# Optimization experiments

Hardware: AMD Instinct MI355X
Metric: run time of the kernel (lower is better)

The kernel has to match this reference:

```python
import jax, jax.numpy as jnp
import numpy as np

BN_EPS = 1e-5


def setup_inputs() -> dict:
    key = jax.random.key(0)
    ks = jax.random.split(key, 9)
    b, c, h, w = 8, 256, 256, 25
    p2_r = jax.random.normal(ks[0], (b, c, h, w), dtype=jnp.float32)
    # message-passing conv weight; scaled so the 25-step recurrence stays bounded
    W_msg = jax.random.normal(ks[1], (256, 256, 1, 9), dtype=jnp.float32) * 0.02
    bn_gamma = jax.random.uniform(ks[2], (256,), dtype=jnp.float32, minval=0.5, maxval=1.5)
    bn_beta = jax.random.normal(ks[3], (256,), dtype=jnp.float32) * 0.1
    bn_mean = jax.random.normal(ks[4], (256,), dtype=jnp.float32) * 0.1
    bn_var = jax.random.uniform(ks[5], (256,), dtype=jnp.float32, minval=0.5, maxval=1.5)
    W_up2 = jax.random.normal(ks[6], (256, 256, 3, 3), dtype=jnp.float32) * (1.0 / np.sqrt(256 * 9))
    W_conv = jax.random.normal(ks[7], (1, 256, 1, 1), dtype=jnp.float32) * (1.0 / np.sqrt(256))
    W_conv2 = jax.random.normal(ks[8], (1, 25, 1, 1), dtype=jnp.float32) * (1.0 / np.sqrt(25))
    return {"p2_r": p2_r, "W_msg": W_msg, "bn_gamma": bn_gamma, "bn_beta": bn_beta,
            "bn_mean": bn_mean, "bn_var": bn_var, "W_up2": W_up2,
            "W_conv": W_conv, "W_conv2": W_conv2}


def r_scnn(x, Wc, reverse):
    # x: [b,c,h,w]. The (1,9) conv with padding (0,4) on width-1 slices only
    # touches the kernel's center tap -> per-step 256x256 matvec recurrence.
    xs = jnp.moveaxis(x, 3, 0)  # [w,b,c,h]
    if reverse:
        xs = xs[::-1]

    def step(carry, xi):
        new = xi + jax.nn.relu(jnp.einsum('oc,bch->boh', Wc, carry))
        return new, new

    _, rest = jax.lax.scan(step, xs[0], xs[1:])
    out = jnp.concatenate([xs[:1], rest], axis=0)[::-1]  # source reverses output order
    return jnp.moveaxis(out, 0, 3)  # [b,c,h,w]


def batchnorm(x, gamma, beta, mean, var):
    inv = gamma / jnp.sqrt(var + BN_EPS)
    return x * inv[None, :, None, None] + (beta - mean * inv)[None, :, None, None]


def upsample_h2(x):
    # bilinear, align_corners=True, size=(2H, W): only height doubles
    b, c, H, W = x.shape
    nh = 2 * H
    pos = jnp.arange(nh, dtype=jnp.float32) * ((H - 1) / (nh - 1))
    i0 = jnp.floor(pos).astype(jnp.int32)
    i1 = jnp.minimum(i0 + 1, H - 1)
    t = (pos - i0.astype(jnp.float32))[None, None, :, None]
    return x[:, :, i0, :] * (1.0 - t) + x[:, :, i1, :] * t


def reference(p2_r, W_msg, bn_gamma, bn_beta, bn_mean, bn_var, W_up2, W_conv, W_conv2):
    Wc = W_msg[:, :, 0, 4]  # effective center tap of the (1,9) conv
    x = r_scnn(p2_r, Wc, reverse=False)
    x = jax.nn.relu(batchnorm(x, bn_gamma, bn_beta, bn_mean, bn_var))
    x = r_scnn(x, Wc, reverse=True)
    x = jax.nn.relu(batchnorm(x, bn_gamma, bn_beta, bn_mean, bn_var))
    x = upsample_h2(x)  # [b,256,2h,w]
    x = jax.lax.conv_general_dilated(x, W_up2, (1, 1), ((1, 1), (1, 1)),
                                     dimension_numbers=('NCHW', 'OIHW', 'NCHW'))
    x = upsample_h2(x)  # [b,256,4h,w]
    x = jnp.einsum('oc,bchw->bohw', W_conv[:, :, 0, 0], x)  # 1x1 conv 256->1
    x = upsample_h2(x)  # [b,1,8h,w]
    x = jnp.swapaxes(x, 1, 3)  # [b,w,8h,1]
    x = jnp.einsum('oc,bchw->bohw', W_conv2[:, :, 0, 0], x)  # 1x1 conv 25->1
    return jax.nn.sigmoid(x)  # [b,1,8h,1]
```

## Files before the change

### kernel.cpp

```cpp
#include <hip/hip_runtime.h>
#include <math.h>


#define NC 8

typedef __attribute__((ext_vector_type(8))) short bf16x8;
typedef __attribute__((ext_vector_type(4))) float f32x4;

__device__ __forceinline__ float relu_(float v) { return fmaxf(v, 0.f); }

__device__ __forceinline__ short f2bf(float f) {
  union { float f; unsigned u; } v; v.f = f;
  unsigned r = (v.u + 0x7fffu + ((v.u >> 16) & 1u)) >> 16;
  return (short)r;
}
__device__ __forceinline__ float bf2f(short s) {
  union { unsigned u; float f; } v;
  v.u = ((unsigned)(unsigned short)s) << 16;
  return v.f;
}
__device__ __forceinline__ unsigned cvtpk(float lo, float hi) {
  unsigned r;
  asm("v_cvt_pk_bf16_f32 %0, %1, %2" : "=v"(r) : "v"(lo), "v"(hi));
  return r;
}
__device__ __forceinline__ float dpp_xor8(float v) {
  int r = __builtin_amdgcn_update_dpp(0, __float_as_int(v), 0x128, 0xf, 0xf, true);
  return __int_as_float(r);
}

__global__ __launch_bounds__(64) void k0_precompute(
    const float* __restrict__ Wmsg, const float* __restrict__ gamma,
    const float* __restrict__ beta, const float* __restrict__ mean,
    const float* __restrict__ var, const float* __restrict__ Wup2,
    const float* __restrict__ Wconv, const float* __restrict__ Wconv2,
    short* __restrict__ WcA, float* __restrict__ A, float* __restrict__ bnp)
{
  const int c = blockIdx.x;
  const int lane = threadIdx.x;

  for (int o = lane; o < 256; o += 64)
    WcA[o * 256 + c] = f2bf(Wmsg[(o * 256 + c) * 9 + 4]);

  const int gtid = c * 64 + lane;
  if (gtid < 256) {
    float inv = gamma[gtid] / sqrtf(var[gtid] + 1e-5f);
    bnp[gtid] = inv;
    bnp[256 + gtid] = beta[gtid] - mean[gtid] * inv;
  }

  float wacc[9];
#pragma unroll
  for (int q = 0; q < 9; ++q) wacc[q] = 0.f;
  for (int o = lane; o < 256; o += 64) {
    float cw = Wconv[o];
    const float* wp = Wup2 + (size_t)(o * 256 + c) * 9;
#pragma unroll
    for (int q = 0; q < 9; ++q) wacc[q] += cw * wp[q];
  }
#pragma unroll
  for (int q = 0; q < 9; ++q) {
    float v = wacc[q];
    v += __shfl_xor(v, 32, 64);
    v += __shfl_xor(v, 16, 64);
    v += __shfl_xor(v, 8, 64);
    v += __shfl_xor(v, 4, 64);
    v += __shfl_xor(v, 2, 64);
    v += __shfl_xor(v, 1, 64);
    wacc[q] = v;
  }
  if (lane == 0) {
    for (int dh = 0; dh < 3; ++dh)
      for (int j = 0; j < 25; ++j) {
        float a = 0.f;
        for (int dw = 0; dw < 3; ++dw) {
          int w = j + 1 - dw;
          if (w >= 0 && w < 25) a += wacc[dh * 3 + dw] * Wconv2[w];
        }
        A[(dh * 25 + j) * 256 + c] = a;
      }
  }
}

__global__ __launch_bounds__(512, 1) void k2_fused(
    const float* __restrict__ X,
    const short* __restrict__ WcA,
    const float* __restrict__ A,
    const float* __restrict__ bnp,
    float* __restrict__ S)
{
  __shared__ short xslab[25 * 8 * 256];
  __shared__ short yz[2][16 * 256];
  __shared__ float red[8][8][3];
  const int tid = threadIdx.x;
  const int wave = tid >> 6;
  const int lane = tid & 63;
  const int n = lane & 15;
  const int nr = n & 7;
  const int g = lane >> 4;
  const bool isz = (n >= 8);
  const int col0 = blockIdx.x * NC;
  const int b = col0 >> 8, h0 = col0 & 255;
  const int obase = wave * 32;
  char* xs = (char*)xslab;
  char* smem = (char*)yz;

  if (lane < 50) {
    int base_[4], sx_[4];
#pragma unroll
    for (int e = 0; e < 4; ++e) {
      int f = 4 * lane + e;
      int rn = f / 25, w = f - rn * 25;
      base_[e] = w * 4096 + rn * 512;
      sx_[e] = ((2 * rn + w) & 15) << 3;
    }
    const float* src0 = X + (size_t)(b * 256 + obase) * 6400 + h0 * 25 + 4 * lane;
#pragma unroll 4
    for (int i = 0; i < 16; ++i) {
      float4 v0 = *(const float4*)(src0 + (size_t)(2 * i) * 6400);
      float4 v1 = *(const float4*)(src0 + (size_t)(2 * i + 1) * 6400);
      unsigned p[4] = {cvtpk(v0.x, v1.x), cvtpk(v0.y, v1.y),
                       cvtpk(v0.z, v1.z), cvtpk(v0.w, v1.w)};
      const int cb = 2 * obase + 4 * i;
#pragma unroll
      for (int e = 0; e < 4; ++e)
        *(unsigned*)(xs + base_[e] + (cb ^ sx_[e])) = p[e];
    }
  }

  f32x4 inv[2], addv[2];
#pragma unroll
  for (int t = 0; t < 2; ++t) {
    inv[t] = *(const f32x4*)(bnp + obase + t * 16 + g * 4);
    addv[t] = *(const f32x4*)(bnp + 256 + obase + t * 16 + g * 4);
  }

  bf16x8 af[2][8];
#pragma unroll
  for (int t = 0; t < 2; ++t)
#pragma unroll
    for (int kk = 0; kk < 8; ++kk)
      af[t][kk] = *(const bf16x8*)(WcA + (obase + t * 16 + n) * 256 + kk * 32 + g * 8);

  const int swz = nr << 4;
  int woff[2], xb[2], roff[8];
#pragma unroll
  for (int t = 0; t < 2; ++t) {
    woff[t] = n * 512 + (((obase + t * 16 + g * 4) * 2) ^ swz);
    xb[t] = nr * 512 + 2 * (obase + t * 16 + g * 4);
  }
#pragma unroll
  for (int kk = 0; kk < 8; ++kk)
    roff[kk] = n * 512 + ((kk * 64 + g * 16) ^ swz);

  __syncthreads();

  {
    const int S0 = ((2 * nr) & 15) << 3;
#pragma unroll
    for (int t = 0; t < 2; ++t) {
      uint2 xq0 = *(const uint2*)(xs + (xb[t] ^ S0));
      if (!isz) {
        *(uint2*)(smem + woff[t]) = xq0;
      } else {
        float zr[4], t2r[4];
        float xv[4] = {bf2f((short)xq0.x), bf2f((short)(xq0.x >> 16)),
                       bf2f((short)xq0.y), bf2f((short)(xq0.y >> 16))};
#pragma unroll
        for (int r = 0; r < 4; ++r) {
          zr[r] = relu_(xv[r] * inv[t][r] + addv[t][r]);
          t2r[r] = relu_(zr[r] * inv[t][r] + addv[t][r]);
        }
        *(uint2*)(smem + woff[t]) = make_uint2(cvtpk(zr[0], zr[1]), cvtpk(zr[2], zr[3]));
        *(uint2*)(xs + (xb[t] ^ S0)) =
            make_uint2(cvtpk(t2r[0], t2r[1]), cvtpk(t2r[2], t2r[3]));
      }
    }
  }

  uint2 xq[2];
  xq[0] = make_uint2(0u, 0u);
  xq[1] = make_uint2(0u, 0u);
  if (!isz) {
    const int S1 = ((2 * nr + 1) & 15) << 3;
#pragma unroll
    for (int t = 0; t < 2; ++t)
      xq[t] = *(const uint2*)(xs + ((xb[t] + 4096) ^ S1));
  }
  __syncthreads();

#pragma unroll 1
  for (int k = 1; k < 25; ++k) {
    const int cur = (k - 1) & 1, nxt = k & 1;

    bf16x8 bfr[8];
#pragma unroll
    for (int kk = 0; kk < 8; ++kk)
      bfr[kk] = *(const bf16x8*)(smem + cur * 8192 + roff[kk]);

    f32x4 accA[2], accB[2];
#pragma unroll
    for (int t = 0; t < 2; ++t) {
      accA[t] = (f32x4){0.f, 0.f, 0.f, 0.f};
      accB[t] = (f32x4){0.f, 0.f, 0.f, 0.f};
    }
    __builtin_amdgcn_s_setprio(1);
#pragma unroll
    for (int kk = 0; kk < 4; ++kk)
#pragma unroll
      for (int t = 0; t < 2; ++t)
        accA[t] = __builtin_amdgcn_mfma_f32_16x16x32_bf16(af[t][kk], bfr[kk], accA[t], 0, 0, 0);
#pragma unroll
    for (int kk = 4; kk < 8; ++kk)
#pragma unroll
      for (int t = 0; t < 2; ++t)
        accB[t] = __builtin_amdgcn_mfma_f32_16x16x32_bf16(af[t][kk], bfr[kk], accB[t], 0, 0, 0);
    __builtin_amdgcn_s_setprio(0);

    float cyv[2][4], ynv[2][4], t1v[2][4], t1s[2][4];
#pragma unroll
    for (int t = 0; t < 2; ++t) {
      f32x4 acc = accA[t] + accB[t];
      float xv[4];
      xv[0] = bf2f((short)xq[t].x);
      xv[1] = bf2f((short)(xq[t].x >> 16));
      xv[2] = bf2f((short)xq[t].y);
      xv[3] = bf2f((short)(xq[t].y >> 16));
#pragma unroll
      for (int r = 0; r < 4; ++r) {
        cyv[t][r] = relu_(acc[r]);
        ynv[t][r] = xv[r] + cyv[t][r];
        t1v[t][r] = relu_(ynv[t][r] * inv[t][r] + addv[t][r]);
      }
    }
#pragma unroll
    for (int t = 0; t < 2; ++t)
#pragma unroll
      for (int r = 0; r < 4; ++r) t1s[t][r] = dpp_xor8(t1v[t][r]);
#pragma unroll
    for (int t = 0; t < 2; ++t) {
      float sel[4], tt2[4];
#pragma unroll
      for (int r = 0; r < 4; ++r) {
        float znew = t1s[t][r] + cyv[t][r];
        tt2[r] = relu_(znew * inv[t][r] + addv[t][r]);
        sel[r] = isz ? znew : ynv[t][r];
      }
      *(uint2*)(smem + nxt * 8192 + woff[t]) =
          make_uint2(cvtpk(sel[0], sel[1]), cvtpk(sel[2], sel[3]));
      if (isz)
        *(uint2*)(xs + ((xb[t] + k * 4096) ^ (((2 * nr + k) & 15) << 3))) =
            make_uint2(cvtpk(tt2[0], tt2[1]), cvtpk(tt2[2], tt2[3]));
    }

    if (k < 24 && !isz) {
      const int Sn = ((2 * nr + k + 1) & 15) << 3;
#pragma unroll
      for (int t = 0; t < 2; ++t)
        xq[t] = *(const uint2*)(xs + ((xb[t] + (k + 1) * 4096) ^ Sn));
    }
    __syncthreads();
  }

  {
    const int kb = (wave == 0) ? 0 : 4 + 3 * (wave - 1);
    const int ke = kb + (wave ? 3 : 4);
    float acc[8][3];
#pragma unroll
    for (int rn = 0; rn < 8; ++rn)
#pragma unroll
      for (int dh = 0; dh < 3; ++dh) acc[rn][dh] = 0.f;

#pragma unroll 1
    for (int k = kb; k < ke; ++k) {
      f32x4 a0 = *(const f32x4*)(A + (0 * 25 + 24 - k) * 256 + 4 * lane);
      f32x4 a1 = *(const f32x4*)(A + (1 * 25 + 24 - k) * 256 + 4 * lane);
      f32x4 a2 = *(const f32x4*)(A + (2 * 25 + 24 - k) * 256 + 4 * lane);
#pragma unroll
      for (int rn = 0; rn < 8; ++rn) {
        int Sp = ((2 * rn + k) & 15) << 3;
        uint2 q = *(const uint2*)(xs + ((k * 4096 + rn * 512 + 8 * lane) ^ Sp));
        float v0 = bf2f((short)q.x), v1 = bf2f((short)(q.x >> 16));
        float v2 = bf2f((short)q.y), v3 = bf2f((short)(q.y >> 16));
#pragma unroll
        for (int dh = 0; dh < 3; ++dh) {
          f32x4 a = dh == 0 ? a0 : (dh == 1 ? a1 : a2);
          float s = acc[rn][dh];
          s = fmaf(a[0], v0, s);
          s = fmaf(a[1], v1, s);
          s = fmaf(a[2], v2, s);
          s = fmaf(a[3], v3, s);
          acc[rn][dh] = s;
        }
      }
    }
#pragma unroll
    for (int rn = 0; rn < 8; ++rn)
#pragma unroll
      for (int dh = 0; dh < 3; ++dh) {
        float v = acc[rn][dh];
        v += __shfl_xor(v, 1);
        v += __shfl_xor(v, 2);
        v += __shfl_xor(v, 4);
        v += __shfl_xor(v, 8);
        v += __shfl_xor(v, 16);
        v += __shfl_xor(v, 32);
        if (lane == 0) red[wave][rn][dh] = v;
      }
  }
  __syncthreads();
  if (tid < 24) {
    int nn = tid / 3, dh = tid % 3;
    float v = 0.f;
#pragma unroll
    for (int ww = 0; ww < 8; ++ww) v += red[ww][nn][dh];
    S[(size_t)(col0 + nn) * 3 + dh] = v;
  }
}

__global__ __launch_bounds__(256) void k34_final(
    const float* __restrict__ S, float* __restrict__ out)
{
  int idx = blockIdx.x * blockDim.x + threadIdx.x;
  if (idx >= 8 * 2048) return;
  int b = idx >> 11, H = idx & 2047;

  auto Pf = [&](int h) -> float {
    float acc = 0.f;
#pragma unroll
    for (int dh = 0; dh < 3; ++dh) {
      int hh = h + dh - 1;
      if (hh < 0 || hh >= 512) continue;
      float pos = hh * (255.0f / 511.0f);
      int i0 = (int)floorf(pos);
      int i1 = min(i0 + 1, 255);
      float t = pos - (float)i0;
      acc += (1.f - t) * S[(size_t)(b * 256 + i0) * 3 + dh]
           + t * S[(size_t)(b * 256 + i1) * 3 + dh];
    }
    return acc;
  };

  float pos3 = H * (1023.0f / 2047.0f);
  int i3 = (int)floorf(pos3);
  int i3b = min(i3 + 1, 1023);
  float t3 = pos3 - (float)i3;

  float v[2];
#pragma unroll
  for (int q = 0; q < 2; ++q) {
    int i = q ? i3b : i3;
    float pos2 = i * (511.0f / 1023.0f);
    int i2 = (int)floorf(pos2);
    int i2b = min(i2 + 1, 511);
    float t2 = pos2 - (float)i2;
    v[q] = (1.f - t2) * Pf(i2) + t2 * Pf(i2b);
  }
  float val = (1.f - t3) * v[0] + t3 * v[1];
  out[idx] = 1.f / (1.f + expf(-val));
}

extern "C" void kernel_launch(void* const* d_in, const int* in_sizes, int n_in,
                              void* d_out, int out_size, void* d_ws, size_t ws_size,
                              hipStream_t stream) {
  (void)in_sizes; (void)n_in; (void)out_size; (void)ws_size;
  const float* p2r    = (const float*)d_in[0];
  const float* Wmsg   = (const float*)d_in[1];
  const float* gamma  = (const float*)d_in[2];
  const float* beta   = (const float*)d_in[3];
  const float* mean   = (const float*)d_in[4];
  const float* var    = (const float*)d_in[5];
  const float* Wup2   = (const float*)d_in[6];
  const float* Wconv  = (const float*)d_in[7];
  const float* Wconv2 = (const float*)d_in[8];
  float* out = (float*)d_out;

  float* ws = (float*)d_ws;
  size_t off = 0;
  short* WcA = (short*)(ws + off); off += 32768;
  float* Abuf = ws + off; off += 19200;
  float* bnp = ws + off;  off += 512;
  float* S = ws + off;    off += 6144;

  k0_precompute<<<256, 64, 0, stream>>>(Wmsg, gamma, beta, mean, var, Wup2,
                                        Wconv, Wconv2, WcA, Abuf, bnp);
  k2_fused<<<256, 512, 0, stream>>>(p2r, (const short*)WcA, Abuf, bnp, S);
  k34_final<<<64, 256, 0, stream>>>(S, out);
}
```

Measured before the change: 52.98 us.

## Load input sequence directly into registers and fully unroll the recurrence

Non-z lanes now load their own 4 channels × 25 timesteps straight from global memory into registers as packed bf16, instead of staging the input through the shared-memory slab. This removes the slab staging pass, the per-step shared-memory reads of x, and one barrier. The z lanes get the x values via a DPP xor-8 exchange. The 25-step loop is fully unrolled so the register arrays can be indexed statically. The cost is about 100 extra VGPRs per thread, which risks lower occupancy or spills, plus unaligned float4 global loads with stride-25 rows that may coalesce less well.

```diff
diff --git a/kernel.cpp b/kernel.cpp
--- a/kernel.cpp
+++ b/kernel.cpp
@@ -6,6 +6,7 @@
 
 typedef __attribute__((ext_vector_type(8))) short bf16x8;
 typedef __attribute__((ext_vector_type(4))) float f32x4;
+typedef __attribute__((ext_vector_type(4), aligned(4))) float f32x4u;
 
 __device__ __forceinline__ float relu_(float v) { return fmaxf(v, 0.f); }
 
@@ -105,26 +106,37 @@
   char* xs = (char*)xslab;
   char* smem = (char*)yz;
 
-  if (lane < 50) {
-    int base_[4], sx_[4];
-#pragma unroll
-    for (int e = 0; e < 4; ++e) {
-      int f = 4 * lane + e;
-      int rn = f / 25, w = f - rn * 25;
-      base_[e] = w * 4096 + rn * 512;
-      sx_[e] = ((2 * rn + w) & 15) << 3;
-    }
-    const float* src0 = X + (size_t)(b * 256 + obase) * 6400 + h0 * 25 + 4 * lane;
-#pragma unroll 4
-    for (int i = 0; i < 16; ++i) {
-      float4 v0 = *(const float4*)(src0 + (size_t)(2 * i) * 6400);
-      float4 v1 = *(const float4*)(src0 + (size_t)(2 * i + 1) * 6400);
-      unsigned p[4] = {cvtpk(v0.x, v1.x), cvtpk(v0.y, v1.y),
-                       cvtpk(v0.z, v1.z), cvtpk(v0.w, v1.w)};
-      const int cb = 2 * obase + 4 * i;
-#pragma unroll
-      for (int e = 0; e < 4; ++e)
-        *(unsigned*)(xs + base_[e] + (cb ^ sx_[e])) = p[e];
+  unsigned pA[2][25], pB[2][25];
+#pragma unroll
+  for (int t = 0; t < 2; ++t)
+#pragma unroll
+    for (int k = 0; k < 25; ++k) { pA[t][k] = 0u; pB[t][k] = 0u; }
+
+  if (!isz) {
+    const int h = h0 + n;
+#pragma unroll
+    for (int t = 0; t < 2; ++t) {
+      const float* r0 =
+          X + ((size_t)(b * 256 + obase + t * 16 + g * 4) * 256 + h) * 25;
+      const float* r1 = r0 + 6400;
+      const float* r2 = r0 + 12800;
+      const float* r3 = r0 + 19200;
+      f32x4u v0[6], v1[6], v2[6], v3[6];
+#pragma unroll
+      for (int q = 0; q < 6; ++q) {
+        v0[q] = *(const f32x4u*)(r0 + 4 * q);
+        v1[q] = *(const f32x4u*)(r1 + 4 * q);
+        v2[q] = *(const f32x4u*)(r2 + 4 * q);
+        v3[q] = *(const f32x4u*)(r3 + 4 * q);
+      }
+      float l0 = r0[24], l1 = r1[24], l2 = r2[24], l3 = r3[24];
+#pragma unroll
+      for (int k = 0; k < 24; ++k) {
+        pA[t][k] = cvtpk(v0[k >> 2][k & 3], v1[k >> 2][k & 3]);
+        pB[t][k] = cvtpk(v2[k >> 2][k & 3], v3[k >> 2][k & 3]);
+      }
+      pA[t][24] = cvtpk(l0, l1);
+      pB[t][24] = cvtpk(l2, l3);
     }
   }
 
@@ -153,43 +165,34 @@
   for (int kk = 0; kk < 8; ++kk)
     roff[kk] = n * 512 + ((kk * 64 + g * 16) ^ swz);
 
-  __syncthreads();
-
   {
-    const int S0 = ((2 * nr) & 15) << 3;
-#pragma unroll
-    for (int t = 0; t < 2; ++t) {
-      uint2 xq0 = *(const uint2*)(xs + (xb[t] ^ S0));
+    const int S0 = 0 ;
+#pragma unroll
+    for (int t = 0; t < 2; ++t) {
+      float x0[4] = {bf2f((short)pA[t][0]), bf2f((short)(pA[t][0] >> 16)),
+                     bf2f((short)pB[t][0]), bf2f((short)(pB[t][0] >> 16))};
+      float px[4];
+#pragma unroll
+      for (int r = 0; r < 4; ++r) px[r] = dpp_xor8(x0[r]);
       if (!isz) {
-        *(uint2*)(smem + woff[t]) = xq0;
+        *(uint2*)(smem + woff[t]) = make_uint2(pA[t][0], pB[t][0]);
       } else {
         float zr[4], t2r[4];
-        float xv[4] = {bf2f((short)xq0.x), bf2f((short)(xq0.x >> 16)),
-                       bf2f((short)xq0.y), bf2f((short)(xq0.y >> 16))};
 #pragma unroll
         for (int r = 0; r < 4; ++r) {
-          zr[r] = relu_(xv[r] * inv[t][r] + addv[t][r]);
+          zr[r] = relu_(px[r] * inv[t][r] + addv[t][r]);
           t2r[r] = relu_(zr[r] * inv[t][r] + addv[t][r]);
         }
         *(uint2*)(smem + woff[t]) = make_uint2(cvtpk(zr[0], zr[1]), cvtpk(zr[2], zr[3]));
-        *(uint2*)(xs + (xb[t] ^ S0)) =
+        *(uint2*)(xs + ((xb[t] + 0) ^ (((2 * nr) & 15) << 3))) =
             make_uint2(cvtpk(t2r[0], t2r[1]), cvtpk(t2r[2], t2r[3]));
       }
     }
-  }
-
-  uint2 xq[2];
-  xq[0] = make_uint2(0u, 0u);
-  xq[1] = make_uint2(0u, 0u);
-  if (!isz) {
-    const int S1 = ((2 * nr + 1) & 15) << 3;
-#pragma unroll
-    for (int t = 0; t < 2; ++t)
-      xq[t] = *(const uint2*)(xs + ((xb[t] + 4096) ^ S1));
+    (void)S0;
   }
   __syncthreads();
 
-#pragma unroll 1
+#pragma unroll
   for (int k = 1; k < 25; ++k) {
     const int cur = (k - 1) & 1, nxt = k & 1;
 
@@ -222,10 +225,10 @@
     for (int t = 0; t < 2; ++t) {
       f32x4 acc = accA[t] + accB[t];
       float xv[4];
-      xv[0] = bf2f((short)xq[t].x);
-      xv[1] = bf2f((short)(xq[t].x >> 16));
-      xv[2] = bf2f((short)xq[t].y);
-      xv[3] = bf2f((short)(xq[t].y >> 16));
+      xv[0] = bf2f((short)pA[t][k]);
+      xv[1] = bf2f((short)(pA[t][k] >> 16));
+      xv[2] = bf2f((short)pB[t][k]);
+      xv[3] = bf2f((short)(pB[t][k] >> 16));
 #pragma unroll
       for (int r = 0; r < 4; ++r) {
         cyv[t][r] = relu_(acc[r]);
@@ -251,13 +254,6 @@
       if (isz)
         *(uint2*)(xs + ((xb[t] + k * 4096) ^ (((2 * nr + k) & 15) << 3))) =
             make_uint2(cvtpk(tt2[0], tt2[1]), cvtpk(tt2[2], tt2[3]));
-    }
-
-    if (k < 24 && !isz) {
-      const int Sn = ((2 * nr + k + 1) & 15) << 3;
-#pragma unroll
-      for (int t = 0; t < 2; ++t)
-        xq[t] = *(const uint2*)(xs + ((xb[t] + (k + 1) * 4096) ^ Sn));
     }
     __syncthreads();
   }
```

Measured after the change: 53.48 us. About the same (+0.9%).
